# Kernel tuning notes

Measured on AMD Instinct MI355X. Metric: run time of the kernel, lower is better.

## Reference

```python
import jax, jax.numpy as jnp
import numpy as np


def _ln(x, g, b, eps=1e-5):
    m = x.mean(-1, keepdims=True)
    v = x.var(-1, keepdims=True)
    return (x - m) / jnp.sqrt(v + eps) * g + b


def setup_inputs() -> dict:
    key = jax.random.key(0)
    ks = iter(jax.random.split(key, 48))
    B, N, H, Ld, L, FF = 2048, 10, 256, 8, 4, 1024
    def w(shape, s=0.02):
        return jax.random.normal(next(ks), shape, jnp.float32) * s
    return dict(
        latent_code=jax.random.normal(next(ks), (B, Ld), jnp.float32),
        target_node_types=jax.random.randint(next(ks), (B, N), 0, 5),
        ce_w1=w((Ld, H)), ce_b1=jnp.zeros(H), ce_g1=jnp.ones(H), ce_be1=jnp.zeros(H),
        ce_w2=w((H, H)), ce_b2=jnp.zeros(H), ce_g2=jnp.ones(H), ce_be2=jnp.zeros(H),
        nc_w1=w((2, H // 4)), nc_b1=jnp.zeros(H // 4), nc_w2=w((H // 4, 3)), nc_b2=jnp.zeros(3),
        type_emb=w((5, H), 1.0), pos_emb=w((N, H), 0.02),
        qkvo_w=w((L, 4, H, H)), qkvo_b=jnp.zeros((L, 4, H)),
        ln_g=jnp.ones((L, 2, H)), ln_b=jnp.zeros((L, 2, H)),
        ffn_w1=w((L, H, FF)), ffn_b1=jnp.zeros((L, FF)),
        ffn_w2=w((L, FF, H)), ffn_b2=jnp.zeros((L, H)),
        out_w=w((H, 5)), out_b=jnp.zeros(5),
        edge_w1=w((2 * H + Ld, H)), edge_b1=jnp.zeros(H),
        edge_w2=w((H, 8)), edge_b2=jnp.zeros(8),
    )


def reference(latent_code, target_node_types,
              ce_w1, ce_b1, ce_g1, ce_be1, ce_w2, ce_b2, ce_g2, ce_be2,
              nc_w1, nc_b1, nc_w2, nc_b2,
              type_emb, pos_emb, qkvo_w, qkvo_b, ln_g, ln_b,
              ffn_w1, ffn_b1, ffn_w2, ffn_b2, out_w, out_b,
              edge_w1, edge_b1, edge_w2, edge_b2):
    B, Ld = latent_code.shape
    N = target_node_types.shape[1]
    H = ce_w1.shape[1]
    L = qkvo_w.shape[0]
    nh = 8
    hd = H // nh

    # context encoder: Linear -> LN -> ReLU -> Linear -> LN
    h0 = jax.nn.relu(_ln(latent_code @ ce_w1 + ce_b1, ce_g1, ce_be1))
    context = _ln(h0 @ ce_w2 + ce_b2, ce_g2, ce_be2)  # [B,H]

    # node count head on latent_code[:, :2]
    node_count_logits = jax.nn.relu(latent_code[:, :2] @ nc_w1 + nc_b1) @ nc_w2 + nc_b2  # [B,3]

    # teacher-forced node embeddings (independent of predictions -> vectorizable)
    ne = type_emb[target_node_types] + pos_emb[:N]          # [B,N,H]
    h = context[:, None, :] + pos_emb[:N]                   # queries [B,N,H]
    mem = jnp.concatenate([context[:, None, :], ne], axis=1)  # keys [B,N+1,H]
    # position i attends to context (k=0) and nodes j<i (k=j+1), i.e. k <= i
    kmask = (jnp.arange(N + 1)[None, :] <= jnp.arange(N)[:, None])  # [N,N+1]
    scale = 1.0 / np.sqrt(hd).astype(np.float32)

    for l in range(L):
        Q = (h @ qkvo_w[l, 0] + qkvo_b[l, 0]).reshape(B, N, nh, hd)
        K = (mem @ qkvo_w[l, 1] + qkvo_b[l, 1]).reshape(B, N + 1, nh, hd)
        V = (mem @ qkvo_w[l, 2] + qkvo_b[l, 2]).reshape(B, N + 1, nh, hd)
        s = jnp.einsum('bnhd,bmhd->bhnm', Q, K) * scale
        s = jnp.where(kmask[None, None], s, jnp.float32(-1e9))
        a = jax.nn.softmax(s, axis=-1)
        o = jnp.einsum('bhnm,bmhd->bnhd', a, V).reshape(B, N, H)
        h = _ln(h + o @ qkvo_w[l, 3] + qkvo_b[l, 3], ln_g[l, 0], ln_b[l, 0])
        f = jax.nn.relu(h @ ffn_w1[l] + ffn_b1[l]) @ ffn_w2[l] + ffn_b2[l]
        h = _ln(h + f, ln_g[l, 1], ln_b[l, 1])

    node_logits = h @ out_w + out_b  # [B,N,5]

    # pairwise edge decoder on (emb_i, emb_j, latent) for i>j, symmetrized
    ei = jnp.broadcast_to(ne[:, :, None, :], (B, N, N, H))
    ej = jnp.broadcast_to(ne[:, None, :, :], (B, N, N, H))
    lat = jnp.broadcast_to(latent_code[:, None, None, :], (B, N, N, Ld))
    feat = jnp.concatenate([ei, ej, lat], axis=-1)  # [B,N,N,2H+Ld]
    elog = jax.nn.relu(feat @ edge_w1 + edge_b1) @ edge_w2 + edge_b2  # [B,N,N,8]
    tril = (jnp.arange(N)[:, None] > jnp.arange(N)[None, :])[None, :, :, None]
    lower = jnp.where(tril, elog, jnp.float32(0.0))
    edge_component_logits = lower + jnp.swapaxes(lower, 1, 2)  # diag stays zero

    return node_logits, node_count_logits, edge_component_logits
```

## Files before the change

kernel.cpp:

```cpp
#include <hip/hip_runtime.h>
#include <hip/hip_bf16.h>

#define BATCH 2048
#define NNODE 10
#define NLAYER 4
#define ROWS_H (BATCH*NNODE)
#define ROWS_M (BATCH*(NNODE+1))

typedef __hip_bfloat16 bf16;
typedef unsigned short u16;
typedef unsigned int u32;
typedef __attribute__((ext_vector_type(8))) short bf16x8;
typedef __attribute__((ext_vector_type(4))) float f32x4;

__device__ __forceinline__ float bfb(u16 u) {
    union { u32 i; float f; } c; c.i = (u32)u << 16; return c.f;
}
__device__ __forceinline__ float bf2f(bf16 x) { return __bfloat162float(x); }
__device__ __forceinline__ bf16 f2bf(float x) { return __float2bfloat16(x); }
__device__ __forceinline__ u16 f2u(float v) {
    bf16 t = f2bf(v); u16 u; __builtin_memcpy(&u, &t, 2); return u;
}
__device__ __forceinline__ void store_out(void* out, int f32o, size_t idx, float v) {
    if (f32o) ((float*)out)[idx] = v; else ((bf16*)out)[idx] = f2bf(v);
}
__device__ __forceinline__ int dflag(const u32* g) { return g[0] == 0x3F800000u; }

#define GLL(src, dst) __builtin_amdgcn_global_load_lds( \
    (const __attribute__((address_space(1))) void*)(src), \
    (__attribute__((address_space(3))) void*)(dst), 16, 0, 0)

#define NT 26
struct CvtArgs { const void* src[NT]; int n[NT]; int off[NT]; };

__global__ __launch_bounds__(256) void cvt_kernel(CvtArgs a, bf16* __restrict__ dst,
                                                  const u32* __restrict__ gptr) {
    int f = dflag(gptr);
    int gid = blockIdx.x * 256 + threadIdx.x;
    int stride = gridDim.x * 256;
    for (int tn = 0; tn < NT; tn++) {
        const void* s = a.src[tn];
        bf16* d = dst + a.off[tn];
        int n = a.n[tn];
        if (f) {
            const float* sf = (const float*)s;
            for (int i = gid; i < n; i += stride) d[i] = f2bf(sf[i]);
        } else {
            const bf16* sb = (const bf16*)s;
            for (int i = gid; i < n; i += stride) d[i] = sb[i];
        }
    }
}

#define NTT 26
struct TTArgs { const void* src[NTT]; int soff[NTT]; int doff[NTT]; int R[NTT]; int Cc[NTT]; };

__global__ __launch_bounds__(256) void tt_kernel(TTArgs a, u16* __restrict__ dst,
                                                 const u32* __restrict__ gptr) {
    int f = dflag(gptr);
    int gid = blockIdx.x * 256 + threadIdx.x;
    int stride = gridDim.x * 256;
    for (int tn = 0; tn < NTT; tn++) {
        int R = a.R[tn], C = a.Cc[tn], n = R * C;
        u16* d = dst + a.doff[tn];
        if (f) {
            const float* s = (const float*)a.src[tn] + a.soff[tn];
            for (int i = gid; i < n; i += stride) {
                int r = i / C, c = i - r * C;
                d[c * R + r] = f2u(s[i]);
            }
        } else {
            const u16* s = (const u16*)a.src[tn] + a.soff[tn];
            for (int i = gid; i < n; i += stride) {
                int r = i / C, c = i - r * C;
                d[c * R + r] = s[i];
            }
        }
    }
}

__device__ __forceinline__ void ln_stats256(float x, float* s_red, float& m, float& var) {
    float v1 = x, v2 = x * x;
    #pragma unroll
    for (int off = 32; off; off >>= 1) {
        v1 += __shfl_down(v1, off, 64);
        v2 += __shfl_down(v2, off, 64);
    }
    int wave = threadIdx.x >> 6, lane = threadIdx.x & 63;
    if (!lane) { s_red[wave] = v1; s_red[4 + wave] = v2; }
    __syncthreads();
    m   = (s_red[0] + s_red[1] + s_red[2] + s_red[3]) * (1.f / 256.f);
    var = (s_red[4] + s_red[5] + s_red[6] + s_red[7]) * (1.f / 256.f) - m * m;
    __syncthreads();
}

__global__ __launch_bounds__(256) void ctx_kernel(
    const bf16* __restrict__ lat_bf, const int* __restrict__ types,
    const bf16* __restrict__ ce_w1, const bf16* __restrict__ ce_b1,
    const bf16* __restrict__ ce_g1, const bf16* __restrict__ ce_be1,
    const bf16* __restrict__ ce_w2, const bf16* __restrict__ ce_b2,
    const bf16* __restrict__ ce_g2, const bf16* __restrict__ ce_be2,
    const bf16* __restrict__ nc_w1, const bf16* __restrict__ nc_b1,
    const bf16* __restrict__ nc_w2, const bf16* __restrict__ nc_b2,
    const bf16* __restrict__ type_emb, const bf16* __restrict__ pos_emb,
    const bf16* __restrict__ edge_w1, const bf16* __restrict__ edge_b1,
    bf16* __restrict__ h, bf16* __restrict__ mem, bf16* __restrict__ ne,
    bf16* __restrict__ rvec, void* __restrict__ out, const u32* __restrict__ gptr)
{
    int b = blockIdx.x;
    int t = threadIdx.x;
    int f32o = dflag(gptr);
    __shared__ float lat[8];
    __shared__ float s_h0[256];
    __shared__ float s_red[8];
    __shared__ float s_nc[64];

    if (t < 8) lat[t] = bf2f(lat_bf[b * 8 + t]);
    __syncthreads();

    float x = bf2f(ce_b1[t]);
    #pragma unroll
    for (int k = 0; k < 8; k++) x += lat[k] * bf2f(ce_w1[k * 256 + t]);
    float m, var;
    ln_stats256(x, s_red, m, var);
    float r = rsqrtf(var + 1e-5f);
    float h0 = fmaxf((x - m) * r * bf2f(ce_g1[t]) + bf2f(ce_be1[t]), 0.f);
    s_h0[t] = h0;
    __syncthreads();

    float x2 = bf2f(ce_b2[t]);
    for (int k = 0; k < 256; k++) x2 += s_h0[k] * bf2f(ce_w2[k * 256 + t]);
    ln_stats256(x2, s_red, m, var);
    r = rsqrtf(var + 1e-5f);
    float ctx = (x2 - m) * r * bf2f(ce_g2[t]) + bf2f(ce_be2[t]);

    mem[(size_t)(b * 11) * 256 + t] = f2bf(ctx);
    for (int n = 0; n < NNODE; n++) {
        float pe = bf2f(pos_emb[n * 256 + t]);
        h[(size_t)(b * NNODE + n) * 256 + t] = f2bf(ctx + pe);
        int ty = types[b * NNODE + n];
        float nv = bf2f(type_emb[ty * 256 + t]) + pe;
        ne[(size_t)(b * NNODE + n) * 256 + t] = f2bf(nv);
        mem[(size_t)(b * 11 + 1 + n) * 256 + t] = f2bf(nv);
    }

    float rv = bf2f(edge_b1[t]);
    #pragma unroll
    for (int k = 0; k < 8; k++) rv += lat[k] * bf2f(edge_w1[(512 + k) * 256 + t]);
    rvec[(size_t)b * 256 + t] = f2bf(rv);

    if (t < 64) {
        float hn = lat[0] * bf2f(nc_w1[t]) + lat[1] * bf2f(nc_w1[64 + t]) + bf2f(nc_b1[t]);
        s_nc[t] = fmaxf(hn, 0.f);
    }
    __syncthreads();
    if (t < 3) {
        float o = bf2f(nc_b2[t]);
        for (int k = 0; k < 64; k++) o += s_nc[k] * bf2f(nc_w2[k * 3 + t]);
        store_out(out, f32o, (size_t)102400 + b * 3 + t, o);
    }
}

__global__ __launch_bounds__(256) void gemm_mfma(
    const u16* __restrict__ A, const u16* __restrict__ Bt,
    const bf16* __restrict__ bias, bf16* __restrict__ C,
    int M, int K, int N, int act)
{
    __shared__ u16 Als[128 * 32];
    __shared__ u16 Bls[128 * 32];
    int t = threadIdx.x;
    int w = t >> 6, l = t & 63;
    int m0 = blockIdx.y * 128, n0 = blockIdx.x * 128;
    int wr = (w >> 1) * 64, wc = (w & 1) * 64;

    int srow = w * 32 + (l >> 2);
    int selem = (l & 3) * 8;
    const u16* Ag = A + (size_t)(m0 + srow) * K + selem;
    const u16* Bg = Bt + (size_t)(n0 + srow) * K + selem;

    f32x4 acc[4][4];
    #pragma unroll
    for (int i = 0; i < 4; i++)
        #pragma unroll
        for (int j = 0; j < 4; j++)
            acc[i][j] = (f32x4){0.f, 0.f, 0.f, 0.f};

    int koff = (l >> 4) * 8;
    int mrow = wr + (l & 15);
    int ncol = wc + (l & 15);

    for (int kt = 0; kt < K; kt += 32) {
        const u16* ag = Ag + kt;
        const u16* bg = Bg + kt;
        GLL(ag, &Als[w * 1024]);
        GLL(ag + (size_t)16 * K, &Als[w * 1024 + 512]);
        GLL(bg, &Bls[w * 1024]);
        GLL(bg + (size_t)16 * K, &Bls[w * 1024 + 512]);
        __syncthreads();

        bf16x8 af[4], bfr[4];
        #pragma unroll
        for (int i = 0; i < 4; i++) {
            af[i]  = *(const bf16x8*)&Als[(mrow + i * 16) * 32 + koff];
            bfr[i] = *(const bf16x8*)&Bls[(ncol + i * 16) * 32 + koff];
        }
        #pragma unroll
        for (int i = 0; i < 4; i++)
            #pragma unroll
            for (int j = 0; j < 4; j++)
                acc[i][j] = __builtin_amdgcn_mfma_f32_16x16x32_bf16(af[i], bfr[j], acc[i][j], 0, 0, 0);
        __syncthreads();
    }

    int rbase = (l >> 4) * 4;
    #pragma unroll
    for (int i = 0; i < 4; i++) {
        int m = m0 + wr + i * 16 + rbase;
        #pragma unroll
        for (int j = 0; j < 4; j++) {
            int n = n0 + wc + j * 16 + (l & 15);
            float bv = bias ? bf2f(bias[n]) : 0.f;
            #pragma unroll
            for (int r = 0; r < 4; r++) {
                float v = acc[i][j][r] + bv;
                if (act) v = fmaxf(v, 0.f);
                C[(size_t)(m + r) * N + n] = f2bf(v);
            }
        }
    }
}

template<int MODE>
__global__ __launch_bounds__(256) void gemm256(
    const u16* __restrict__ A, const u16* __restrict__ Bt,
    const bf16* __restrict__ bias, const bf16* __restrict__ g,
    const bf16* __restrict__ be, u16* __restrict__ hio,
    u16* __restrict__ C, int K)
{
    __shared__ u16 Asl[32 * 32];
    __shared__ u16 Bsl[256 * 32];
    __shared__ float lnp[2][4][32];
    int t = threadIdx.x, w = t >> 6, l = t & 63, q = l >> 4, l15 = l & 15;
    int m0 = blockIdx.x * 32;

    const u16* Ag = A + (size_t)(m0 + w * 16 + (l >> 2)) * K + (l & 3) * 8;
    const u16* Bg = Bt + (size_t)(w * 64 + (l >> 2)) * K + (l & 3) * 8;

    f32x4 acc[2][4];
    #pragma unroll
    for (int i = 0; i < 2; i++)
        #pragma unroll
        for (int j = 0; j < 4; j++)
            acc[i][j] = (f32x4){0.f, 0.f, 0.f, 0.f};

    for (int kt = 0; kt < K; kt += 32) {
        if (w < 2) GLL(Ag + kt, &Asl[w * 512]);
        #pragma unroll
        for (int s = 0; s < 4; s++)
            GLL(Bg + kt + (size_t)(s * 16) * K, &Bsl[w * 2048 + s * 512]);
        __syncthreads();
        bf16x8 af[2], bfr[4];
        #pragma unroll
        for (int i = 0; i < 2; i++)
            af[i] = *(const bf16x8*)&Asl[(i * 16 + l15) * 32 + q * 8];
        #pragma unroll
        for (int j = 0; j < 4; j++)
            bfr[j] = *(const bf16x8*)&Bsl[(w * 64 + j * 16 + l15) * 32 + q * 8];
        #pragma unroll
        for (int i = 0; i < 2; i++)
            #pragma unroll
            for (int j = 0; j < 4; j++)
                acc[i][j] = __builtin_amdgcn_mfma_f32_16x16x32_bf16(af[i], bfr[j], acc[i][j], 0, 0, 0);
        __syncthreads();
    }

    float bv[4];
    #pragma unroll
    for (int j = 0; j < 4; j++) bv[j] = bf2f(bias[w * 64 + j * 16 + l15]);

    if (MODE == 0) {
        #pragma unroll
        for (int i = 0; i < 2; i++)
            #pragma unroll
            for (int r = 0; r < 4; r++) {
                int row = m0 + i * 16 + q * 4 + r;
                #pragma unroll
                for (int j = 0; j < 4; j++)
                    C[(size_t)row * 256 + w * 64 + j * 16 + l15] = f2u(acc[i][j][r] + bv[j]);
            }
    } else {
        float gv[4], bev[4];
        #pragma unroll
        for (int j = 0; j < 4; j++) {
            gv[j] = bf2f(g[w * 64 + j * 16 + l15]);
            bev[j] = bf2f(be[w * 64 + j * 16 + l15]);
        }
        #pragma unroll
        for (int i = 0; i < 2; i++)
            #pragma unroll
            for (int r = 0; r < 4; r++) {
                int row = m0 + i * 16 + q * 4 + r;
                float s = 0.f, s2 = 0.f;
                #pragma unroll
                for (int j = 0; j < 4; j++) {
                    float xv = acc[i][j][r] + bv[j] + bfb(hio[(size_t)row * 256 + w * 64 + j * 16 + l15]);
                    acc[i][j][r] = xv; s += xv; s2 += xv * xv;
                }
                #pragma unroll
                for (int d = 1; d < 16; d <<= 1) {
                    s  += __shfl_xor(s, d, 64);
                    s2 += __shfl_xor(s2, d, 64);
                }
                if (l15 == 0) {
                    lnp[0][w][i * 16 + q * 4 + r] = s;
                    lnp[1][w][i * 16 + q * 4 + r] = s2;
                }
            }
        __syncthreads();
        #pragma unroll
        for (int i = 0; i < 2; i++)
            #pragma unroll
            for (int r = 0; r < 4; r++) {
                int lr = i * 16 + q * 4 + r;
                float S  = lnp[0][0][lr] + lnp[0][1][lr] + lnp[0][2][lr] + lnp[0][3][lr];
                float S2 = lnp[1][0][lr] + lnp[1][1][lr] + lnp[1][2][lr] + lnp[1][3][lr];
                float mean = S * (1.f / 256.f);
                float var = S2 * (1.f / 256.f) - mean * mean;
                float rstd = rsqrtf(var + 1e-5f);
                #pragma unroll
                for (int j = 0; j < 4; j++)
                    hio[(size_t)(m0 + lr) * 256 + w * 64 + j * 16 + l15] =
                        f2u((acc[i][j][r] - mean) * rstd * gv[j] + bev[j]);
            }
    }
}

__global__ __launch_bounds__(256) void ffn_kernel(
    u16* __restrict__ h, const u16* __restrict__ W1T, const u16* __restrict__ W2T,
    const bf16* __restrict__ b1, const bf16* __restrict__ b2,
    const bf16* __restrict__ g, const bf16* __restrict__ be)
{
    __shared__ u16 Asl[32 * 268];
    __shared__ u16 W1s[128 * 32];
    __shared__ u16 mids[32 * 140];
    __shared__ u16 W2s[256 * 32];
    __shared__ float lnp[2][4][32];

    int t = threadIdx.x, w = t >> 6, l = t & 63, q = l >> 4, l15 = l & 15;
    int m0 = blockIdx.x * 32;

    {
        int row = t >> 3, seg = (t & 7) * 32;
        const u16* src = h + (size_t)(m0 + row) * 256 + seg;
        u16* dst = &Asl[row * 268 + seg];
        #pragma unroll
        for (int u = 0; u < 4; u++)
            *(uint4*)(dst + u * 8) = *(const uint4*)(src + u * 8);
    }

    f32x4 accO[2][4];
    #pragma unroll
    for (int i = 0; i < 2; i++)
        #pragma unroll
        for (int j = 0; j < 4; j++)
            accO[i][j] = (f32x4){0.f, 0.f, 0.f, 0.f};
    __syncthreads();

    for (int c = 0; c < 8; c++) {
        f32x4 accM[2][2];
        #pragma unroll
        for (int i = 0; i < 2; i++) { accM[i][0] = (f32x4){0,0,0,0}; accM[i][1] = (f32x4){0,0,0,0}; }

        for (int kt = 0; kt < 256; kt += 32) {
            const u16* src = W1T + (size_t)(c * 128 + w * 32 + (l >> 2)) * 256 + kt + (l & 3) * 8;
            GLL(src, &W1s[w * 1024]);
            GLL(src + (size_t)16 * 256, &W1s[w * 1024 + 512]);
            __syncthreads();
            bf16x8 af[2], bfm[2];
            #pragma unroll
            for (int i = 0; i < 2; i++)
                af[i] = *(const bf16x8*)&Asl[(i * 16 + l15) * 268 + kt + q * 8];
            #pragma unroll
            for (int j = 0; j < 2; j++)
                bfm[j] = *(const bf16x8*)&W1s[(w * 32 + j * 16 + l15) * 32 + q * 8];
            #pragma unroll
            for (int i = 0; i < 2; i++)
                #pragma unroll
                for (int j = 0; j < 2; j++)
                    accM[i][j] = __builtin_amdgcn_mfma_f32_16x16x32_bf16(af[i], bfm[j], accM[i][j], 0, 0, 0);
            __syncthreads();
        }
        float b1v[2];
        #pragma unroll
        for (int j = 0; j < 2; j++) b1v[j] = bf2f(b1[c * 128 + w * 32 + j * 16 + l15]);
        #pragma unroll
        for (int i = 0; i < 2; i++)
            #pragma unroll
            for (int j = 0; j < 2; j++)
                #pragma unroll
                for (int r = 0; r < 4; r++) {
                    int row = i * 16 + q * 4 + r, col = w * 32 + j * 16 + l15;
                    mids[row * 140 + col] = f2u(fmaxf(accM[i][j][r] + b1v[j], 0.f));
                }
        __syncthreads();

        for (int kt2 = 0; kt2 < 4; kt2++) {
            const u16* src = W2T + (size_t)(w * 64 + (l >> 2)) * 1024 + c * 128 + kt2 * 32 + (l & 3) * 8;
            #pragma unroll
            for (int s = 0; s < 4; s++)
                GLL(src + (size_t)(s * 16) * 1024, &W2s[w * 2048 + s * 512]);
            __syncthreads();
            bf16x8 am[2], bo[4];
            #pragma unroll
            for (int i = 0; i < 2; i++)
                am[i] = *(const bf16x8*)&mids[(i * 16 + l15) * 140 + kt2 * 32 + q * 8];
            #pragma unroll
            for (int j = 0; j < 4; j++)
                bo[j] = *(const bf16x8*)&W2s[(w * 64 + j * 16 + l15) * 32 + q * 8];
            #pragma unroll
            for (int i = 0; i < 2; i++)
                #pragma unroll
                for (int j = 0; j < 4; j++)
                    accO[i][j] = __builtin_amdgcn_mfma_f32_16x16x32_bf16(am[i], bo[j], accO[i][j], 0, 0, 0);
            __syncthreads();
        }
    }

    float b2v[4], gv[4], bev[4];
    #pragma unroll
    for (int j = 0; j < 4; j++) {
        int col = w * 64 + j * 16 + l15;
        b2v[j] = bf2f(b2[col]); gv[j] = bf2f(g[col]); bev[j] = bf2f(be[col]);
    }
    #pragma unroll
    for (int i = 0; i < 2; i++)
        #pragma unroll
        for (int r = 0; r < 4; r++) {
            int row = i * 16 + q * 4 + r;
            float s = 0.f, s2 = 0.f;
            #pragma unroll
            for (int j = 0; j < 4; j++) {
                float xv = accO[i][j][r] + b2v[j] + bfb(Asl[row * 268 + w * 64 + j * 16 + l15]);
                accO[i][j][r] = xv; s += xv; s2 += xv * xv;
            }
            #pragma unroll
            for (int d = 1; d < 16; d <<= 1) {
                s  += __shfl_xor(s, d, 64);
                s2 += __shfl_xor(s2, d, 64);
            }
            if (l15 == 0) { lnp[0][w][row] = s; lnp[1][w][row] = s2; }
        }
    __syncthreads();
    #pragma unroll
    for (int i = 0; i < 2; i++)
        #pragma unroll
        for (int r = 0; r < 4; r++) {
            int lr = i * 16 + q * 4 + r;
            float S  = lnp[0][0][lr] + lnp[0][1][lr] + lnp[0][2][lr] + lnp[0][3][lr];
            float S2 = lnp[1][0][lr] + lnp[1][1][lr] + lnp[1][2][lr] + lnp[1][3][lr];
            float mean = S * (1.f / 256.f);
            float var = S2 * (1.f / 256.f) - mean * mean;
            float rstd = rsqrtf(var + 1e-5f);
            #pragma unroll
            for (int j = 0; j < 4; j++)
                h[(size_t)(m0 + lr) * 256 + w * 64 + j * 16 + l15] =
                    f2u((accO[i][j][r] - mean) * rstd * gv[j] + bev[j]);
        }
}

__global__ __launch_bounds__(256) void attn_kernel(
    const bf16* __restrict__ Qb, const bf16* __restrict__ KVb,
    bf16* __restrict__ Ob)
{
    int b = blockIdx.x;
    int t = threadIdx.x;
    __shared__ float Qs[10 * 256];
    __shared__ float Ks[11 * 256];
    __shared__ float S[880];

    for (int i = 0; i < 10; i++) Qs[i * 256 + t] = bf2f(Qb[(size_t)(b * 10 + i) * 256 + t]);
    for (int k = 0; k < 11; k++) Ks[k * 256 + t] = bf2f(KVb[(size_t)(b * 11 + k) * 512 + t]);
    __syncthreads();

    const float scale = 0.17677669529663687f;
    for (int e = t; e < 880; e += 256) {
        int head = e / 110, rem = e % 110, i = rem / 11, k = rem % 11;
        if (k <= i) {
            const float* qp = &Qs[i * 256 + head * 32];
            const float* kp = &Ks[k * 256 + head * 32];
            float s = 0.f;
            #pragma unroll
            for (int d = 0; d < 32; d++) s += qp[d] * kp[d];
            S[e] = s * scale;
        }
    }
    __syncthreads();
    if (t < 80) {
        int head = t / 10, i = t % 10;
        float* row = &S[head * 110 + i * 11];
        float mx = -1e30f;
        for (int k = 0; k <= i; k++) mx = fmaxf(mx, row[k]);
        float sum = 0.f;
        for (int k = 0; k <= i; k++) { float e = __expf(row[k] - mx); row[k] = e; sum += e; }
        float inv = 1.f / sum;
        for (int k = 0; k <= i; k++) row[k] *= inv;
    }
    __syncthreads();

    int head = t >> 5;
    float o[10] = {0.f, 0.f, 0.f, 0.f, 0.f, 0.f, 0.f, 0.f, 0.f, 0.f};
    for (int k = 0; k < 11; k++) {
        float v = bf2f(KVb[(size_t)(b * 11 + k) * 512 + 256 + t]);
        for (int i = k; i < 10; i++) o[i] += S[head * 110 + i * 11 + k] * v;
    }
    for (int i = 0; i < 10; i++) Ob[(size_t)(b * 10 + i) * 256 + t] = f2bf(o[i]);
}

__global__ __launch_bounds__(256) void outhead_kernel(
    const bf16* __restrict__ h, const bf16* __restrict__ w,
    const bf16* __restrict__ b, void* __restrict__ out, const u32* __restrict__ gptr)
{
    int f32o = dflag(gptr);
    int wv = threadIdx.x >> 6, l = threadIdx.x & 63;
    size_t row = (size_t)blockIdx.x * 4 + wv;
    ushort4 hv = *(const ushort4*)((const u16*)h + row * 256 + l * 4);
    float x[4] = {bfb(hv.x), bfb(hv.y), bfb(hv.z), bfb(hv.w)};
    float a[5] = {0.f, 0.f, 0.f, 0.f, 0.f};
    #pragma unroll
    for (int c = 0; c < 4; c++) {
        #pragma unroll
        for (int o = 0; o < 5; o++) a[o] += x[c] * bf2f(w[(l * 4 + c) * 5 + o]);
    }
    #pragma unroll
    for (int off = 32; off; off >>= 1)
        #pragma unroll
        for (int o = 0; o < 5; o++) a[o] += __shfl_xor(a[o], off, 64);
    if (!l)
        #pragma unroll
        for (int o = 0; o < 5; o++)
            store_out(out, f32o, row * 5 + o, a[o] + bf2f(b[o]));
}

__global__ __launch_bounds__(256) void edge_kernel(
    const bf16* __restrict__ PQ, const bf16* __restrict__ rvec,
    const bf16* __restrict__ w2, const bf16* __restrict__ b2,
    void* __restrict__ out, const u32* __restrict__ gptr)
{
    int f32o = dflag(gptr);
    int t = threadIdx.x, w = t >> 6, l = t & 63;
    int b = blockIdx.x * 4 + w;
    const size_t ebase = 108544;

    __shared__ u16 Pl[4][10 * 260];
    __shared__ u16 Ql[4][10 * 260];
    __shared__ u16 Rl[4][256];
    __shared__ float Wl[256 * 8];

    const u16* pq = (const u16*)PQ + (size_t)b * 10 * 512;
    #pragma unroll
    for (int i = 0; i < 10; i++) {
        ushort4 pv = *(const ushort4*)(pq + i * 512 + l * 4);
        ushort4 qv = *(const ushort4*)(pq + i * 512 + 256 + l * 4);
        *(ushort4*)&Pl[w][i * 260 + l * 4] = pv;
        *(ushort4*)&Ql[w][i * 260 + l * 4] = qv;
    }
    *(ushort4*)&Rl[w][l * 4] = *(const ushort4*)((const u16*)rvec + (size_t)b * 256 + l * 4);
    {
        const u16* wp = (const u16*)w2 + t * 8;
        #pragma unroll
        for (int o = 0; o < 8; o++) Wl[t * 8 + o] = bfb(wp[o]);
    }
    __syncthreads();

    if (l >= 45 && l < 55) {
        int i = l - 45;
        size_t o0 = ebase + ((size_t)(b * 10 + i) * 10 + i) * 8;
        if (f32o) {
            float4 z = {0.f, 0.f, 0.f, 0.f};
            *(float4*)((float*)out + o0) = z;
            *(float4*)((float*)out + o0 + 4) = z;
        } else {
            uint4 z = {0u, 0u, 0u, 0u};
            *(uint4*)((u16*)out + o0) = z;
        }
    }
    if (l < 45) {
        int i = 1;
        while (i * (i + 1) / 2 <= l) i++;
        int j = l - i * (i - 1) / 2;
        float acc[8] = {0.f, 0.f, 0.f, 0.f, 0.f, 0.f, 0.f, 0.f};
        const u16* Pp = &Pl[w][i * 260];
        const u16* Qp = &Ql[w][j * 260];
        const u16* Rp = &Rl[w][0];
        for (int c = 0; c < 256; c += 4) {
            ushort4 pv = *(const ushort4*)(Pp + c);
            ushort4 qv = *(const ushort4*)(Qp + c);
            ushort4 rv = *(const ushort4*)(Rp + c);
            float hc[4];
            hc[0] = fmaxf(bfb(pv.x) + bfb(qv.x) + bfb(rv.x), 0.f);
            hc[1] = fmaxf(bfb(pv.y) + bfb(qv.y) + bfb(rv.y), 0.f);
            hc[2] = fmaxf(bfb(pv.z) + bfb(qv.z) + bfb(rv.z), 0.f);
            hc[3] = fmaxf(bfb(pv.w) + bfb(qv.w) + bfb(rv.w), 0.f);
            #pragma unroll
            for (int cc = 0; cc < 4; cc++) {
                const float* wp = &Wl[(c + cc) * 8];
                #pragma unroll
                for (int o = 0; o < 8; o++) acc[o] += hc[cc] * wp[o];
            }
        }
        float r8[8];
        #pragma unroll
        for (int o = 0; o < 8; o++) r8[o] = acc[o] + bf2f(b2[o]);
        size_t o0 = ebase + ((size_t)(b * 10 + i) * 10 + j) * 8;
        size_t o1 = ebase + ((size_t)(b * 10 + j) * 10 + i) * 8;
        if (f32o) {
            float4 v0 = {r8[0], r8[1], r8[2], r8[3]};
            float4 v1 = {r8[4], r8[5], r8[6], r8[7]};
            *(float4*)((float*)out + o0) = v0; *(float4*)((float*)out + o0 + 4) = v1;
            *(float4*)((float*)out + o1) = v0; *(float4*)((float*)out + o1 + 4) = v1;
        } else {
            uint4 pk;
            pk.x = (u32)f2u(r8[0]) | ((u32)f2u(r8[1]) << 16);
            pk.y = (u32)f2u(r8[2]) | ((u32)f2u(r8[3]) << 16);
            pk.z = (u32)f2u(r8[4]) | ((u32)f2u(r8[5]) << 16);
            pk.w = (u32)f2u(r8[6]) | ((u32)f2u(r8[7]) << 16);
            *(uint4*)((u16*)out + o0) = pk;
            *(uint4*)((u16*)out + o1) = pk;
        }
    }
}

extern "C" void kernel_launch(void* const* d_in, const int* in_sizes, int n_in,
                              void* d_out, int out_size, void* d_ws, size_t ws_size,
                              hipStream_t stream) {
    const int* types = (const int*)d_in[1];
    const u32* gptr = (const u32*)d_in[18];

    static const int kIdx[NT] = {0,2,3,4,5,6,7,8,9,10,11,12,13,14,15,17,18,19,21,23,24,25,26,27,28,29};
    static const int kSz[NT]  = {16384,2048,256,256,256,65536,256,256,256,128,64,192,3,1280,2560,
                                 4096,2048,2048,4096,1024,1280,5,133120,256,2048,8};
    bf16* wbf = (bf16*)d_ws;

    CvtArgs ca;
    const bf16* cv[30];
    int off = 0;
    for (int i = 0; i < NT; i++) {
        ca.src[i] = d_in[kIdx[i]];
        ca.n[i] = kSz[i];
        ca.off[i] = off;
        cv[kIdx[i]] = wbf + off;
        off = (off + kSz[i] + 7) & ~7;
    }

    size_t wtbase_e = ((size_t)off + 127) & ~(size_t)127;
    u16* wt = (u16*)wbf + wtbase_e;
    TTArgs ta;
    int tn = 0;
    for (int l = 0; l < NLAYER; l++) {
        int base = l * 786432;
        for (int z = 0; z < 4; z++) {
            static const int dz[4] = {0, 65536, 131072, 196608};
            ta.src[tn] = d_in[16]; ta.soff[tn] = (l * 4 + z) * 65536;
            ta.doff[tn] = base + dz[z]; ta.R[tn] = 256; ta.Cc[tn] = 256; tn++;
        }
        ta.src[tn] = d_in[20]; ta.soff[tn] = l * 262144; ta.doff[tn] = base + 262144; ta.R[tn] = 256;  ta.Cc[tn] = 1024; tn++;
        ta.src[tn] = d_in[22]; ta.soff[tn] = l * 262144; ta.doff[tn] = base + 524288; ta.R[tn] = 1024; ta.Cc[tn] = 256;  tn++;
    }
    ta.src[tn] = d_in[26]; ta.soff[tn] = 0;     ta.doff[tn] = 3145728;         ta.R[tn] = 256; ta.Cc[tn] = 256; tn++;
    ta.src[tn] = d_in[26]; ta.soff[tn] = 65536; ta.doff[tn] = 3145728 + 65536; ta.R[tn] = 256; ta.Cc[tn] = 256; tn++;

    size_t actbase_e = wtbase_e + 3276800 + 128;

    size_t EH = (size_t)ROWS_H * 256, EM = (size_t)ROWS_M * 256;
    bf16* p = (bf16*)wbf + actbase_e;
    bf16* h    = p; p += EH;
    bf16* mem  = p; p += EM;
    bf16* ne   = p; p += EH;
    bf16* rvec = p; p += (size_t)BATCH * 256;
    bf16* span = p;
    bf16* qbuf = span;
    bf16* kvbuf = qbuf + EH;
    bf16* obuf = kvbuf + (size_t)ROWS_M * 512;
    bf16* pqbuf = span;

    cvt_kernel<<<256, 256, 0, stream>>>(ca, wbf, gptr);
    tt_kernel<<<512, 256, 0, stream>>>(ta, wt, gptr);

    ctx_kernel<<<BATCH, 256, 0, stream>>>(
        cv[0], types, cv[2], cv[3], cv[4], cv[5], cv[6], cv[7], cv[8], cv[9],
        cv[10], cv[11], cv[12], cv[13], cv[14], cv[15], cv[26], cv[27],
        h, mem, ne, rvec, d_out, gptr);

    for (int l = 0; l < NLAYER; l++) {
        const u16* qT  = wt + (size_t)l * 786432;
        const u16* kvT = qT + 65536;
        const u16* oT  = qT + 196608;
        const u16* f1T = qT + 262144;
        const u16* f2T = qT + 524288;
        const bf16* bq  = cv[17] + (size_t)(l * 4 + 0) * 256;
        const bf16* bkv = cv[17] + (size_t)(l * 4 + 1) * 256;
        const bf16* bo  = cv[17] + (size_t)(l * 4 + 3) * 256;
        const bf16* g1 = cv[18] + (size_t)(l * 2) * 256, *be1 = cv[19] + (size_t)(l * 2) * 256;
        const bf16* g2 = cv[18] + (size_t)(l * 2 + 1) * 256, *be2 = cv[19] + (size_t)(l * 2 + 1) * 256;

        gemm256<0><<<ROWS_H / 32, 256, 0, stream>>>((const u16*)h, qT, bq, nullptr, nullptr,
                                                    nullptr, (u16*)qbuf, 256);
        gemm_mfma<<<dim3(4, ROWS_M / 128), 256, 0, stream>>>((const u16*)mem, kvT, bkv, kvbuf, ROWS_M, 256, 512, 0);
        attn_kernel<<<BATCH, 256, 0, stream>>>(qbuf, kvbuf, obuf);
        gemm256<1><<<ROWS_H / 32, 256, 0, stream>>>((const u16*)obuf, oT, bo, g1, be1,
                                                    (u16*)h, nullptr, 256);
        ffn_kernel<<<ROWS_H / 32, 256, 0, stream>>>((u16*)h, f1T, f2T,
                                                    cv[21] + (size_t)l * 1024, cv[23] + (size_t)l * 256,
                                                    g2, be2);
    }

    outhead_kernel<<<ROWS_H / 4, 256, 0, stream>>>(h, cv[24], cv[25], d_out, gptr);

    gemm_mfma<<<dim3(4, ROWS_H / 128), 256, 0, stream>>>((const u16*)ne, wt + 3145728, nullptr, pqbuf, ROWS_H, 256, 512, 0);
    edge_kernel<<<BATCH / 4, 256, 0, stream>>>(pqbuf, rvec, cv[28], cv[29], d_out, gptr);
}
```

Measured before the change: 684.7 us.

## Unfuse FFN into two tiled GEMM launches and vectorize attention loads

Removes the fused FFN kernel, which kept each 32-row block's 1024-wide intermediate in shared memory, and replaces it with a gemm_mfma launch (bias+ReLU) that writes the intermediate to a global buffer, followed by gemm256 with residual+LayerNorm over K=1024. This aims for better tiling and weight reuse in the large GEMMs, paying extra global traffic for the intermediate. It also vectorizes the bf16 loads in the attention kernel into shared memory and replaces the divides in the transpose kernel with shifts and masks.

```diff
diff --git a/kernel.cpp b/kernel.cpp
--- a/kernel.cpp
+++ b/kernel.cpp
@@ -53,7 +53,7 @@
 }
 
 #define NTT 26
-struct TTArgs { const void* src[NTT]; int soff[NTT]; int doff[NTT]; int R[NTT]; int Cc[NTT]; };
+struct TTArgs { const void* src[NTT]; int soff[NTT]; int doff[NTT]; int lR[NTT]; int lC[NTT]; };
 
 __global__ __launch_bounds__(256) void tt_kernel(TTArgs a, u16* __restrict__ dst,
                                                  const u32* __restrict__ gptr) {
@@ -61,19 +61,20 @@
     int gid = blockIdx.x * 256 + threadIdx.x;
     int stride = gridDim.x * 256;
     for (int tn = 0; tn < NTT; tn++) {
-        int R = a.R[tn], C = a.Cc[tn], n = R * C;
+        int lR = a.lR[tn], lC = a.lC[tn];
+        int n = 1 << (lR + lC), Cm = (1 << lC) - 1;
         u16* d = dst + a.doff[tn];
         if (f) {
             const float* s = (const float*)a.src[tn] + a.soff[tn];
             for (int i = gid; i < n; i += stride) {
-                int r = i / C, c = i - r * C;
-                d[c * R + r] = f2u(s[i]);
+                int r = i >> lC, c = i & Cm;
+                d[(c << lR) + r] = f2u(s[i]);
             }
         } else {
             const u16* s = (const u16*)a.src[tn] + a.soff[tn];
             for (int i = gid; i < n; i += stride) {
-                int r = i / C, c = i - r * C;
-                d[c * R + r] = s[i];
+                int r = i >> lC, c = i & Cm;
+                d[(c << lR) + r] = s[i];
             }
         }
     }
@@ -335,139 +336,6 @@
     }
 }
 
-__global__ __launch_bounds__(256) void ffn_kernel(
-    u16* __restrict__ h, const u16* __restrict__ W1T, const u16* __restrict__ W2T,
-    const bf16* __restrict__ b1, const bf16* __restrict__ b2,
-    const bf16* __restrict__ g, const bf16* __restrict__ be)
-{
-    __shared__ u16 Asl[32 * 268];
-    __shared__ u16 W1s[128 * 32];
-    __shared__ u16 mids[32 * 140];
-    __shared__ u16 W2s[256 * 32];
-    __shared__ float lnp[2][4][32];
-
-    int t = threadIdx.x, w = t >> 6, l = t & 63, q = l >> 4, l15 = l & 15;
-    int m0 = blockIdx.x * 32;
-
-    {
-        int row = t >> 3, seg = (t & 7) * 32;
-        const u16* src = h + (size_t)(m0 + row) * 256 + seg;
-        u16* dst = &Asl[row * 268 + seg];
-        #pragma unroll
-        for (int u = 0; u < 4; u++)
-            *(uint4*)(dst + u * 8) = *(const uint4*)(src + u * 8);
-    }
-
-    f32x4 accO[2][4];
-    #pragma unroll
-    for (int i = 0; i < 2; i++)
-        #pragma unroll
-        for (int j = 0; j < 4; j++)
-            accO[i][j] = (f32x4){0.f, 0.f, 0.f, 0.f};
-    __syncthreads();
-
-    for (int c = 0; c < 8; c++) {
-        f32x4 accM[2][2];
-        #pragma unroll
-        for (int i = 0; i < 2; i++) { accM[i][0] = (f32x4){0,0,0,0}; accM[i][1] = (f32x4){0,0,0,0}; }
-
-        for (int kt = 0; kt < 256; kt += 32) {
-            const u16* src = W1T + (size_t)(c * 128 + w * 32 + (l >> 2)) * 256 + kt + (l & 3) * 8;
-            GLL(src, &W1s[w * 1024]);
-            GLL(src + (size_t)16 * 256, &W1s[w * 1024 + 512]);
-            __syncthreads();
-            bf16x8 af[2], bfm[2];
-            #pragma unroll
-            for (int i = 0; i < 2; i++)
-                af[i] = *(const bf16x8*)&Asl[(i * 16 + l15) * 268 + kt + q * 8];
-            #pragma unroll
-            for (int j = 0; j < 2; j++)
-                bfm[j] = *(const bf16x8*)&W1s[(w * 32 + j * 16 + l15) * 32 + q * 8];
-            #pragma unroll
-            for (int i = 0; i < 2; i++)
-                #pragma unroll
-                for (int j = 0; j < 2; j++)
-                    accM[i][j] = __builtin_amdgcn_mfma_f32_16x16x32_bf16(af[i], bfm[j], accM[i][j], 0, 0, 0);
-            __syncthreads();
-        }
-        float b1v[2];
-        #pragma unroll
-        for (int j = 0; j < 2; j++) b1v[j] = bf2f(b1[c * 128 + w * 32 + j * 16 + l15]);
-        #pragma unroll
-        for (int i = 0; i < 2; i++)
-            #pragma unroll
-            for (int j = 0; j < 2; j++)
-                #pragma unroll
-                for (int r = 0; r < 4; r++) {
-                    int row = i * 16 + q * 4 + r, col = w * 32 + j * 16 + l15;
-                    mids[row * 140 + col] = f2u(fmaxf(accM[i][j][r] + b1v[j], 0.f));
-                }
-        __syncthreads();
-
-        for (int kt2 = 0; kt2 < 4; kt2++) {
-            const u16* src = W2T + (size_t)(w * 64 + (l >> 2)) * 1024 + c * 128 + kt2 * 32 + (l & 3) * 8;
-            #pragma unroll
-            for (int s = 0; s < 4; s++)
-                GLL(src + (size_t)(s * 16) * 1024, &W2s[w * 2048 + s * 512]);
-            __syncthreads();
-            bf16x8 am[2], bo[4];
-            #pragma unroll
-            for (int i = 0; i < 2; i++)
-                am[i] = *(const bf16x8*)&mids[(i * 16 + l15) * 140 + kt2 * 32 + q * 8];
-            #pragma unroll
-            for (int j = 0; j < 4; j++)
-                bo[j] = *(const bf16x8*)&W2s[(w * 64 + j * 16 + l15) * 32 + q * 8];
-            #pragma unroll
-            for (int i = 0; i < 2; i++)
-                #pragma unroll
-                for (int j = 0; j < 4; j++)
-                    accO[i][j] = __builtin_amdgcn_mfma_f32_16x16x32_bf16(am[i], bo[j], accO[i][j], 0, 0, 0);
-            __syncthreads();
-        }
-    }
-
-    float b2v[4], gv[4], bev[4];
-    #pragma unroll
-    for (int j = 0; j < 4; j++) {
-        int col = w * 64 + j * 16 + l15;
-        b2v[j] = bf2f(b2[col]); gv[j] = bf2f(g[col]); bev[j] = bf2f(be[col]);
-    }
-    #pragma unroll
-    for (int i = 0; i < 2; i++)
-        #pragma unroll
-        for (int r = 0; r < 4; r++) {
-            int row = i * 16 + q * 4 + r;
-            float s = 0.f, s2 = 0.f;
-            #pragma unroll
-            for (int j = 0; j < 4; j++) {
-                float xv = accO[i][j][r] + b2v[j] + bfb(Asl[row * 268 + w * 64 + j * 16 + l15]);
-                accO[i][j][r] = xv; s += xv; s2 += xv * xv;
-            }
-            #pragma unroll
-            for (int d = 1; d < 16; d <<= 1) {
-                s  += __shfl_xor(s, d, 64);
-                s2 += __shfl_xor(s2, d, 64);
-            }
-            if (l15 == 0) { lnp[0][w][row] = s; lnp[1][w][row] = s2; }
-        }
-    __syncthreads();
-    #pragma unroll
-    for (int i = 0; i < 2; i++)
-        #pragma unroll
-        for (int r = 0; r < 4; r++) {
-            int lr = i * 16 + q * 4 + r;
-            float S  = lnp[0][0][lr] + lnp[0][1][lr] + lnp[0][2][lr] + lnp[0][3][lr];
-            float S2 = lnp[1][0][lr] + lnp[1][1][lr] + lnp[1][2][lr] + lnp[1][3][lr];
-            float mean = S * (1.f / 256.f);
-            float var = S2 * (1.f / 256.f) - mean * mean;
-            float rstd = rsqrtf(var + 1e-5f);
-            #pragma unroll
-            for (int j = 0; j < 4; j++)
-                h[(size_t)(m0 + lr) * 256 + w * 64 + j * 16 + l15] =
-                    f2u((accO[i][j][r] - mean) * rstd * gv[j] + bev[j]);
-        }
-}
-
 __global__ __launch_bounds__(256) void attn_kernel(
     const bf16* __restrict__ Qb, const bf16* __restrict__ KVb,
     bf16* __restrict__ Ob)
@@ -478,8 +346,20 @@
     __shared__ float Ks[11 * 256];
     __shared__ float S[880];
 
-    for (int i = 0; i < 10; i++) Qs[i * 256 + t] = bf2f(Qb[(size_t)(b * 10 + i) * 256 + t]);
-    for (int k = 0; k < 11; k++) Ks[k * 256 + t] = bf2f(KVb[(size_t)(b * 11 + k) * 512 + t]);
+    const u16* Qu = (const u16*)Qb + (size_t)b * 2560;
+    for (int e = t; e < 640; e += 256) {
+        ushort4 v = *(const ushort4*)(Qu + e * 4);
+        int base = e * 4;
+        Qs[base] = bfb(v.x); Qs[base + 1] = bfb(v.y);
+        Qs[base + 2] = bfb(v.z); Qs[base + 3] = bfb(v.w);
+    }
+    const u16* KVu = (const u16*)KVb + (size_t)b * 11 * 512;
+    for (int e = t; e < 704; e += 256) {
+        int k = e >> 6, off = (e & 63) * 4;
+        ushort4 v = *(const ushort4*)(KVu + (size_t)k * 512 + off);
+        float* dst = &Ks[k * 256 + off];
+        dst[0] = bfb(v.x); dst[1] = bfb(v.y); dst[2] = bfb(v.z); dst[3] = bfb(v.w);
+    }
     __syncthreads();
 
     const float scale = 0.17677669529663687f;
@@ -661,13 +541,13 @@
         for (int z = 0; z < 4; z++) {
             static const int dz[4] = {0, 65536, 131072, 196608};
             ta.src[tn] = d_in[16]; ta.soff[tn] = (l * 4 + z) * 65536;
-            ta.doff[tn] = base + dz[z]; ta.R[tn] = 256; ta.Cc[tn] = 256; tn++;
-        }
-        ta.src[tn] = d_in[20]; ta.soff[tn] = l * 262144; ta.doff[tn] = base + 262144; ta.R[tn] = 256;  ta.Cc[tn] = 1024; tn++;
-        ta.src[tn] = d_in[22]; ta.soff[tn] = l * 262144; ta.doff[tn] = base + 524288; ta.R[tn] = 1024; ta.Cc[tn] = 256;  tn++;
-    }
-    ta.src[tn] = d_in[26]; ta.soff[tn] = 0;     ta.doff[tn] = 3145728;         ta.R[tn] = 256; ta.Cc[tn] = 256; tn++;
-    ta.src[tn] = d_in[26]; ta.soff[tn] = 65536; ta.doff[tn] = 3145728 + 65536; ta.R[tn] = 256; ta.Cc[tn] = 256; tn++;
+            ta.doff[tn] = base + dz[z]; ta.lR[tn] = 8; ta.lC[tn] = 8; tn++;
+        }
+        ta.src[tn] = d_in[20]; ta.soff[tn] = l * 262144; ta.doff[tn] = base + 262144; ta.lR[tn] = 8;  ta.lC[tn] = 10; tn++;
+        ta.src[tn] = d_in[22]; ta.soff[tn] = l * 262144; ta.doff[tn] = base + 524288; ta.lR[tn] = 10; ta.lC[tn] = 8;  tn++;
+    }
+    ta.src[tn] = d_in[26]; ta.soff[tn] = 0;     ta.doff[tn] = 3145728;         ta.lR[tn] = 8; ta.lC[tn] = 8; tn++;
+    ta.src[tn] = d_in[26]; ta.soff[tn] = 65536; ta.doff[tn] = 3145728 + 65536; ta.lR[tn] = 8; ta.lC[tn] = 8; tn++;
 
     size_t actbase_e = wtbase_e + 3276800 + 128;
 
@@ -681,6 +561,7 @@
     bf16* qbuf = span;
     bf16* kvbuf = qbuf + EH;
     bf16* obuf = kvbuf + (size_t)ROWS_M * 512;
+    bf16* fbuf = span;
     bf16* pqbuf = span;
 
     cvt_kernel<<<256, 256, 0, stream>>>(ca, wbf, gptr);
@@ -709,9 +590,11 @@
         attn_kernel<<<BATCH, 256, 0, stream>>>(qbuf, kvbuf, obuf);
         gemm256<1><<<ROWS_H / 32, 256, 0, stream>>>((const u16*)obuf, oT, bo, g1, be1,
                                                     (u16*)h, nullptr, 256);
-        ffn_kernel<<<ROWS_H / 32, 256, 0, stream>>>((u16*)h, f1T, f2T,
-                                                    cv[21] + (size_t)l * 1024, cv[23] + (size_t)l * 256,
-                                                    g2, be2);
+        gemm_mfma<<<dim3(8, ROWS_H / 128), 256, 0, stream>>>((const u16*)h, f1T,
+                                                    cv[21] + (size_t)l * 1024, fbuf, ROWS_H, 256, 1024, 1);
+        gemm256<1><<<ROWS_H / 32, 256, 0, stream>>>((const u16*)fbuf, f2T,
+                                                    cv[23] + (size_t)l * 256, g2, be2,
+                                                    (u16*)h, nullptr, 1024);
     }
 
     outhead_kernel<<<ROWS_H / 4, 256, 0, stream>>>(h, cv[24], cv[25], d_out, gptr);
```

Measured after the change: 749.6 us. 1.09x slower.

## Batch all layers' K/V projections of memory into one GEMM before the loop

Applied to the files above, without the earlier changes.

Since the memory tensor is constant across layers, the K/V projections for all four layers are computed in one wide GEMM (N=2048) up front, and attention reads its layer's slice with a 2048-element stride. Weights are relaid out so that KV weights for all layers are contiguous and a concatenated bias vector is built by a small kernel. The transpose kernel uses shifts and masks instead of integer division, and the attention loads are vectorized. This trades per-layer launches for one larger GEMM and a bigger activation buffer with strided reads.

```diff
diff --git a/kernel.cpp b/kernel.cpp
--- a/kernel.cpp
+++ b/kernel.cpp
@@ -6,6 +6,7 @@
 #define NLAYER 4
 #define ROWS_H (BATCH*NNODE)
 #define ROWS_M (BATCH*(NNODE+1))
+#define KVSTR 2048
 
 typedef __hip_bfloat16 bf16;
 typedef unsigned short u16;
@@ -53,7 +54,7 @@
 }
 
 #define NTT 26
-struct TTArgs { const void* src[NTT]; int soff[NTT]; int doff[NTT]; int R[NTT]; int Cc[NTT]; };
+struct TTArgs { const void* src[NTT]; int soff[NTT]; int doff[NTT]; int lR[NTT]; int lC[NTT]; };
 
 __global__ __launch_bounds__(256) void tt_kernel(TTArgs a, u16* __restrict__ dst,
                                                  const u32* __restrict__ gptr) {
@@ -61,21 +62,31 @@
     int gid = blockIdx.x * 256 + threadIdx.x;
     int stride = gridDim.x * 256;
     for (int tn = 0; tn < NTT; tn++) {
-        int R = a.R[tn], C = a.Cc[tn], n = R * C;
+        int lR = a.lR[tn], lC = a.lC[tn];
+        int n = 1 << (lR + lC), Cm = (1 << lC) - 1;
         u16* d = dst + a.doff[tn];
         if (f) {
             const float* s = (const float*)a.src[tn] + a.soff[tn];
             for (int i = gid; i < n; i += stride) {
-                int r = i / C, c = i - r * C;
-                d[c * R + r] = f2u(s[i]);
+                int r = i >> lC, c = i & Cm;
+                d[(c << lR) + r] = f2u(s[i]);
             }
         } else {
             const u16* s = (const u16*)a.src[tn] + a.soff[tn];
             for (int i = gid; i < n; i += stride) {
-                int r = i / C, c = i - r * C;
-                d[c * R + r] = s[i];
-            }
-        }
+                int r = i >> lC, c = i & Cm;
+                d[(c << lR) + r] = s[i];
+            }
+        }
+    }
+}
+
+__global__ __launch_bounds__(256) void kvbias_kernel(const bf16* __restrict__ qb,
+                                                     bf16* __restrict__ dst) {
+    int t = blockIdx.x * 256 + threadIdx.x;
+    if (t < 2048) {
+        int l = t >> 9, c = t & 511;
+        dst[t] = qb[(l * 4 + 1) * 256 + c];
     }
 }
 
@@ -478,8 +489,20 @@
     __shared__ float Ks[11 * 256];
     __shared__ float S[880];
 
-    for (int i = 0; i < 10; i++) Qs[i * 256 + t] = bf2f(Qb[(size_t)(b * 10 + i) * 256 + t]);
-    for (int k = 0; k < 11; k++) Ks[k * 256 + t] = bf2f(KVb[(size_t)(b * 11 + k) * 512 + t]);
+    const u16* Qu = (const u16*)Qb + (size_t)b * 2560;
+    for (int e = t; e < 640; e += 256) {
+        ushort4 v = *(const ushort4*)(Qu + e * 4);
+        int base = e * 4;
+        Qs[base] = bfb(v.x); Qs[base + 1] = bfb(v.y);
+        Qs[base + 2] = bfb(v.z); Qs[base + 3] = bfb(v.w);
+    }
+    const u16* KVu = (const u16*)KVb + (size_t)b * 11 * KVSTR;
+    for (int e = t; e < 704; e += 256) {
+        int k = e >> 6, off = (e & 63) * 4;
+        ushort4 v = *(const ushort4*)(KVu + (size_t)k * KVSTR + off);
+        float* dst = &Ks[k * 256 + off];
+        dst[0] = bfb(v.x); dst[1] = bfb(v.y); dst[2] = bfb(v.z); dst[3] = bfb(v.w);
+    }
     __syncthreads();
 
     const float scale = 0.17677669529663687f;
@@ -510,7 +533,7 @@
     int head = t >> 5;
     float o[10] = {0.f, 0.f, 0.f, 0.f, 0.f, 0.f, 0.f, 0.f, 0.f, 0.f};
     for (int k = 0; k < 11; k++) {
-        float v = bf2f(KVb[(size_t)(b * 11 + k) * 512 + 256 + t]);
+        float v = bf2f(((const bf16*)KVb)[(size_t)(b * 11 + k) * KVSTR + 256 + t]);
         for (int i = k; i < 10; i++) o[i] += S[head * 110 + i * 11 + k] * v;
     }
     for (int i = 0; i < 10; i++) Ob[(size_t)(b * 10 + i) * 256 + t] = f2bf(o[i]);
@@ -654,33 +677,41 @@
 
     size_t wtbase_e = ((size_t)off + 127) & ~(size_t)127;
     u16* wt = (u16*)wbf + wtbase_e;
+    const int PERL = 655360;
+    const int KVBASE = 4 * PERL;
+    const int PQBASE = KVBASE + 524288;
     TTArgs ta;
     int tn = 0;
     for (int l = 0; l < NLAYER; l++) {
-        int base = l * 786432;
-        for (int z = 0; z < 4; z++) {
-            static const int dz[4] = {0, 65536, 131072, 196608};
-            ta.src[tn] = d_in[16]; ta.soff[tn] = (l * 4 + z) * 65536;
-            ta.doff[tn] = base + dz[z]; ta.R[tn] = 256; ta.Cc[tn] = 256; tn++;
-        }
-        ta.src[tn] = d_in[20]; ta.soff[tn] = l * 262144; ta.doff[tn] = base + 262144; ta.R[tn] = 256;  ta.Cc[tn] = 1024; tn++;
-        ta.src[tn] = d_in[22]; ta.soff[tn] = l * 262144; ta.doff[tn] = base + 524288; ta.R[tn] = 1024; ta.Cc[tn] = 256;  tn++;
-    }
-    ta.src[tn] = d_in[26]; ta.soff[tn] = 0;     ta.doff[tn] = 3145728;         ta.R[tn] = 256; ta.Cc[tn] = 256; tn++;
-    ta.src[tn] = d_in[26]; ta.soff[tn] = 65536; ta.doff[tn] = 3145728 + 65536; ta.R[tn] = 256; ta.Cc[tn] = 256; tn++;
-
-    size_t actbase_e = wtbase_e + 3276800 + 128;
+        int base = l * PERL;
+        ta.src[tn] = d_in[16]; ta.soff[tn] = (l * 4 + 0) * 65536;
+        ta.doff[tn] = base; ta.lR[tn] = 8; ta.lC[tn] = 8; tn++;
+        ta.src[tn] = d_in[16]; ta.soff[tn] = (l * 4 + 3) * 65536;
+        ta.doff[tn] = base + 65536; ta.lR[tn] = 8; ta.lC[tn] = 8; tn++;
+        ta.src[tn] = d_in[20]; ta.soff[tn] = l * 262144; ta.doff[tn] = base + 131072; ta.lR[tn] = 8;  ta.lC[tn] = 10; tn++;
+        ta.src[tn] = d_in[22]; ta.soff[tn] = l * 262144; ta.doff[tn] = base + 393216; ta.lR[tn] = 10; ta.lC[tn] = 8;  tn++;
+        ta.src[tn] = d_in[16]; ta.soff[tn] = (l * 4 + 1) * 65536;
+        ta.doff[tn] = KVBASE + l * 131072; ta.lR[tn] = 8; ta.lC[tn] = 8; tn++;
+        ta.src[tn] = d_in[16]; ta.soff[tn] = (l * 4 + 2) * 65536;
+        ta.doff[tn] = KVBASE + l * 131072 + 65536; ta.lR[tn] = 8; ta.lC[tn] = 8; tn++;
+    }
+    ta.src[tn] = d_in[26]; ta.soff[tn] = 0;     ta.doff[tn] = PQBASE;         ta.lR[tn] = 8; ta.lC[tn] = 8; tn++;
+    ta.src[tn] = d_in[26]; ta.soff[tn] = 65536; ta.doff[tn] = PQBASE + 65536; ta.lR[tn] = 8; ta.lC[tn] = 8; tn++;
+
+    size_t actbase_e = wtbase_e + 3801088 + 128;
 
     size_t EH = (size_t)ROWS_H * 256, EM = (size_t)ROWS_M * 256;
     bf16* p = (bf16*)wbf + actbase_e;
-    bf16* h    = p; p += EH;
-    bf16* mem  = p; p += EM;
-    bf16* ne   = p; p += EH;
-    bf16* rvec = p; p += (size_t)BATCH * 256;
-    bf16* span = p;
+    bf16* h      = p; p += EH;
+    bf16* mem    = p; p += EM;
+    bf16* ne     = p; p += EH;
+    bf16* rvec   = p; p += (size_t)BATCH * 256;
+    bf16* kvbias = p; p += 2048;
+    bf16* span   = p; p += (size_t)ROWS_H * 1024;
+    bf16* kv_all = p;
     bf16* qbuf = span;
-    bf16* kvbuf = qbuf + EH;
-    bf16* obuf = kvbuf + (size_t)ROWS_M * 512;
+    bf16* obuf = span + EH;
+    bf16* fbuf = span;
     bf16* pqbuf = span;
 
     cvt_kernel<<<256, 256, 0, stream>>>(ca, wbf, gptr);
@@ -690,23 +721,24 @@
         cv[0], types, cv[2], cv[3], cv[4], cv[5], cv[6], cv[7], cv[8], cv[9],
         cv[10], cv[11], cv[12], cv[13], cv[14], cv[15], cv[26], cv[27],
         h, mem, ne, rvec, d_out, gptr);
+    kvbias_kernel<<<8, 256, 0, stream>>>(cv[17], kvbias);
+
+    gemm_mfma<<<dim3(16, ROWS_M / 128), 256, 0, stream>>>(
+        (const u16*)mem, wt + KVBASE, kvbias, kv_all, ROWS_M, 256, 2048, 0);
 
     for (int l = 0; l < NLAYER; l++) {
-        const u16* qT  = wt + (size_t)l * 786432;
-        const u16* kvT = qT + 65536;
-        const u16* oT  = qT + 196608;
-        const u16* f1T = qT + 262144;
-        const u16* f2T = qT + 524288;
-        const bf16* bq  = cv[17] + (size_t)(l * 4 + 0) * 256;
-        const bf16* bkv = cv[17] + (size_t)(l * 4 + 1) * 256;
-        const bf16* bo  = cv[17] + (size_t)(l * 4 + 3) * 256;
+        const u16* qT  = wt + (size_t)l * PERL;
+        const u16* oT  = qT + 65536;
+        const u16* f1T = qT + 131072;
+        const u16* f2T = qT + 393216;
+        const bf16* bq = cv[17] + (size_t)(l * 4 + 0) * 256;
+        const bf16* bo = cv[17] + (size_t)(l * 4 + 3) * 256;
         const bf16* g1 = cv[18] + (size_t)(l * 2) * 256, *be1 = cv[19] + (size_t)(l * 2) * 256;
         const bf16* g2 = cv[18] + (size_t)(l * 2 + 1) * 256, *be2 = cv[19] + (size_t)(l * 2 + 1) * 256;
 
         gemm256<0><<<ROWS_H / 32, 256, 0, stream>>>((const u16*)h, qT, bq, nullptr, nullptr,
                                                     nullptr, (u16*)qbuf, 256);
-        gemm_mfma<<<dim3(4, ROWS_M / 128), 256, 0, stream>>>((const u16*)mem, kvT, bkv, kvbuf, ROWS_M, 256, 512, 0);
-        attn_kernel<<<BATCH, 256, 0, stream>>>(qbuf, kvbuf, obuf);
+        attn_kernel<<<BATCH, 256, 0, stream>>>(qbuf, kv_all + (size_t)l * 512, obuf);
         gemm256<1><<<ROWS_H / 32, 256, 0, stream>>>((const u16*)obuf, oT, bo, g1, be1,
                                                     (u16*)h, nullptr, 256);
         ffn_kernel<<<ROWS_H / 32, 256, 0, stream>>>((u16*)h, f1T, f2T,
@@ -716,6 +748,6 @@
 
     outhead_kernel<<<ROWS_H / 4, 256, 0, stream>>>(h, cv[24], cv[25], d_out, gptr);
 
-    gemm_mfma<<<dim3(4, ROWS_H / 128), 256, 0, stream>>>((const u16*)ne, wt + 3145728, nullptr, pqbuf, ROWS_H, 256, 512, 0);
+    gemm_mfma<<<dim3(4, ROWS_H / 128), 256, 0, stream>>>((const u16*)ne, wt + PQBASE, nullptr, pqbuf, ROWS_H, 256, 512, 0);
     edge_kernel<<<BATCH / 4, 256, 0, stream>>>(pqbuf, rvec, cv[28], cv[29], d_out, gptr);
 }
```

New measurement: 675.4 us. Within noise of the previous version (-1.4%).
